# Kernel optimization log

Measured on AMD Instinct MI355X. Metric: run time of the kernel, lower is better.

## Reference

```python
import jax, jax.numpy as jnp
import numpy as np

B, L, F, D, T = 8, 400, 128, 256, 256
H = D + T            # deberta hidden_size = transfo_dim + dense_dim
NH = 8               # num_attention_heads
HD = H // NH         # head dim
BUCKETS = 600        # position_buckets == max_relative_positions
P = 2 * BUCKETS      # rel-embedding table rows

def mish(x):
    return x * jnp.tanh(jax.nn.softplus(x))

def layer_norm(x, g, b, eps=1e-7):
    m = x.mean(-1, keepdims=True)
    v = jnp.var(x, axis=-1, keepdims=True)
    return (x - m) / jnp.sqrt(v + eps) * g + b

def _rel_buckets(n, bucket=BUCKETS, max_pos=BUCKETS):
    # DeBERTa-v2 build_relative_position + make_log_bucket_position (static, numpy)
    ids = np.arange(n)
    rel = ids[:, None] - ids[None, :]
    mid = bucket // 2
    sign = np.sign(rel)
    abs_pos = np.where((rel < mid) & (rel > -mid), mid - 1, np.abs(rel))
    log_pos = np.ceil(np.log(abs_pos / mid) / np.log((max_pos - 1) / mid) * (mid - 1)) + mid
    bpos = np.where(abs_pos <= mid, rel, (log_pos * sign).astype(np.int64))
    c2p = np.clip(bpos + bucket, 0, 2 * bucket - 1).astype(np.int32)
    p2c = np.clip(-bpos + bucket, 0, 2 * bucket - 1).astype(np.int32)
    return jnp.asarray(c2p), jnp.asarray(p2c)

def _encoder(feats, mask, c2p_pos, p2c_pos, p):
    # one DebertaV2 layer with disentangled attention (share_att_key=True, pos_att_type=[c2p,p2c])
    (rel_emb, rel_g, rel_b, wq, bq, wk, bk, wv, bv,
     wo, bo, ln1g, ln1b, wi, bi, wout, bout, ln2g, ln2b) = p
    Bq, Lq, _ = feats.shape
    rel = layer_norm(rel_emb, rel_g, rel_b)                       # norm_rel_ebd='layer_norm'
    q = (feats @ wq + bq).reshape(Bq, Lq, NH, HD)
    k = (feats @ wk + bk).reshape(Bq, Lq, NH, HD)
    v = (feats @ wv + bv).reshape(Bq, Lq, NH, HD)
    pq = (rel @ wq + bq).reshape(P, NH, HD)                       # shared att key/query projs
    pk = (rel @ wk + bk).reshape(P, NH, HD)
    scale = np.float32(1.0 / np.sqrt(HD * 3))                     # scale_factor = 1 + 2 pos terms
    scores = jnp.einsum('blhd,bmhd->bhlm', q, k) * scale
    idx = jnp.arange(Lq)[:, None]
    c2p = jnp.einsum('blhd,phd->bhlp', q, pk)                     # [B,h,L,P]
    scores = scores + c2p[:, :, idx, c2p_pos] * scale             # gather c2p bias
    p2c = jnp.einsum('bmhd,phd->bhmp', k, pq)                     # [B,h,L,P]
    scores = scores + jnp.swapaxes(p2c[:, :, idx, p2c_pos], -1, -2) * scale
    valid = (mask[:, None, :, None] != 0) & (mask[:, None, None, :] != 0)
    scores = jnp.where(valid, scores, jnp.finfo(scores.dtype).min)
    probs = jax.nn.softmax(scores, axis=-1)
    ctx = jnp.einsum('bhlm,bmhd->blhd', probs, v).reshape(Bq, Lq, H)
    h1 = layer_norm(ctx @ wo + bo + feats, ln1g, ln1b)            # SelfOutput (residual)
    inter = mish(h1 @ wi + bi)                                    # intermediate, act=Mish
    return layer_norm(inter @ wout + bout, ln2g, ln2b)            # custom Output: skip residual, dim T

def _att_pool(x, w):
    xw = x * w
    return xw.sum(1) / (w.sum(1) + 1e-6), xw.max(1)

def _forward(x, w_mlp, b_mlp, w_cnn, b_cnn, rel_emb, rel_g, rel_b, wq, bq, wk, bk, wv, bv,
             wo, bo, ln1g, ln1b, wi, bi, wout, bout, ln2g, ln2b,
             w_bow1, b_bow1, w_bow2, b_bow2, w_ext1, b_ext1, w_ext2, b_ext2,
             w_org1, b_org1, w_org2, b_org2):
    f1 = mish(x @ w_mlp + b_mlp)                                  # [B,L,D]
    f2 = jax.nn.relu(jax.lax.conv_general_dilated(
        f1, w_cnn, (1,), 'SAME', dimension_numbers=('NWC', 'WIO', 'NWC')) + b_cnn)
    feats = jnp.concatenate([f1, f2], -1)                         # [B,L,H]
    kidney = x[:, :, 2:4].max(-1)
    masks = jnp.stack([x[:, :, 4], kidney, x[:, :, 0], x[:, :, 1]])  # bowel,kidney,liver,spleen [4,B,L]
    c2p_pos, p2c_pos = _rel_buckets(x.shape[1])
    params = (rel_emb, rel_g, rel_b, wq, bq, wk, bk, wv, bv,
              wo, bo, ln1g, ln1b, wi, bi, wout, bout, ln2g, ln2b)
    outs = jax.vmap(lambda m, pp: _encoder(feats, m, c2p_pos, p2c_pos, pp))(masks, params)  # [4,B,L,T]
    att, mx = jax.vmap(_att_pool)(outs, masks[..., None])         # [4,B,T] each
    pooled = jnp.concatenate([att, mx], -1)                       # [4,B,2T]
    mean = feats.mean(1)
    fmax = feats.max(1)
    lb = mish(pooled[0] @ w_bow1 + b_bow1) @ w_bow2 + b_bow2      # [B,1]
    le = mish(jnp.concatenate([mean, fmax], -1) @ w_ext1 + b_ext1) @ w_ext2 + b_ext2  # [B,1]
    ho = mish(jnp.einsum('obf,ofd->obd', pooled[1:], w_org1) + b_org1[:, None])
    lo = jnp.einsum('obd,odc->obc', ho, w_org2) + b_org2[:, None]  # [3,B,3] kidney,liver,spleen
    logits = jnp.concatenate([lb, le, lo[0], lo[1], lo[2]], -1)   # [B,11]
    return logits, jnp.zeros(x.shape[0], x.dtype)

def setup_inputs() -> dict:
    key = jax.random.key(0)
    ks = iter(jax.random.split(key, 64))
    nrm = lambda shape: jax.random.normal(next(ks), shape, jnp.float32) * 0.02
    inp = {}
    inp['x'] = jax.random.uniform(next(ks), (B, L, F), jnp.float32)  # positive: used as soft masks
    inp['w_mlp'] = nrm((F, D)); inp['b_mlp'] = jnp.zeros((D,), jnp.float32)
    inp['w_cnn'] = nrm((3, D, T)); inp['b_cnn'] = jnp.zeros((T,), jnp.float32)
    inp['rel_emb'] = nrm((4, P, H))
    inp['rel_g'] = jnp.ones((4, H), jnp.float32); inp['rel_b'] = jnp.zeros((4, H), jnp.float32)
    for n in ['wq', 'wk', 'wv', 'wo', 'wi']:
        inp[n] = nrm((4, H, H))
    for n in ['bq', 'bk', 'bv', 'bo', 'bi']:
        inp[n] = jnp.zeros((4, H), jnp.float32)
    inp['wout'] = nrm((4, H, T)); inp['bout'] = jnp.zeros((4, T), jnp.float32)
    inp['ln1g'] = jnp.ones((4, H), jnp.float32); inp['ln1b'] = jnp.zeros((4, H), jnp.float32)
    inp['ln2g'] = jnp.ones((4, T), jnp.float32); inp['ln2b'] = jnp.zeros((4, T), jnp.float32)
    inp['w_bow1'] = nrm((2 * T, D)); inp['b_bow1'] = jnp.zeros((D,), jnp.float32)
    inp['w_bow2'] = nrm((D, 1)); inp['b_bow2'] = jnp.zeros((1,), jnp.float32)
    inp['w_ext1'] = nrm((2 * H, D)); inp['b_ext1'] = jnp.zeros((D,), jnp.float32)
    inp['w_ext2'] = nrm((D, 1)); inp['b_ext2'] = jnp.zeros((1,), jnp.float32)
    inp['w_org1'] = nrm((3, 2 * T, D)); inp['b_org1'] = jnp.zeros((3, D), jnp.float32)
    inp['w_org2'] = nrm((3, D, 3)); inp['b_org2'] = jnp.zeros((3, 3), jnp.float32)
    return inp

def reference(x, w_mlp, b_mlp, w_cnn, b_cnn, rel_emb, rel_g, rel_b, wq, bq, wk, bk, wv, bv,
              wo, bo, ln1g, ln1b, wi, bi, wout, bout, ln2g, ln2b,
              w_bow1, b_bow1, w_bow2, b_bow2, w_ext1, b_ext1, w_ext2, b_ext2,
              w_org1, b_org1, w_org2, b_org2):
    return _forward(x, w_mlp, b_mlp, w_cnn, b_cnn, rel_emb, rel_g, rel_b, wq, bq, wk, bk, wv, bv,
                    wo, bo, ln1g, ln1b, wi, bi, wout, bout, ln2g, ln2b,
                    w_bow1, b_bow1, w_bow2, b_bow2, w_ext1, b_ext1, w_ext2, b_ext2,
                    w_org1, b_org1, w_org2, b_org2)
```

## Files before the change

### kernel.cpp

```cpp
#include <hip/hip_runtime.h>
#include <math.h>


typedef __attribute__((ext_vector_type(8))) short bf16x8;
typedef __attribute__((ext_vector_type(4))) float f32x4;
typedef __attribute__((ext_vector_type(4))) unsigned int u32x4;
typedef __attribute__((ext_vector_type(4))) unsigned short us4;

__device__ __forceinline__ float mishf(float x) {
    float sp = fmaxf(x, 0.f) + log1pf(expf(-fabsf(x)));
    return x * tanhf(sp);
}

__device__ __forceinline__ unsigned short f2bf(float f) {
    unsigned int u = __float_as_uint(f);
    u = (u + 0x7fffu + ((u >> 16) & 1u)) >> 16;
    return (unsigned short)u;
}
__device__ __forceinline__ float bf2f(unsigned short h) {
    return __uint_as_float(((unsigned int)h) << 16);
}

__device__ __forceinline__ void gll16(const unsigned short* g, unsigned short* l) {
    __builtin_amdgcn_global_load_lds(
        (const __attribute__((address_space(1))) void*)g,
        (__attribute__((address_space(3))) void*)l, 16, 0, 0);
}

template<int EPI>
__global__ __launch_bounds__(256) void gemm_bias(
    const float* __restrict__ A, const float* __restrict__ Bm,
    const float* __restrict__ bias, float* __restrict__ C2,
    unsigned short* __restrict__ fhi, unsigned short* __restrict__ flo,
    int M, int N, int K, int ldc)
{
    __shared__ float As[16][68];
    __shared__ float Bs[16][68];
    int bm = blockIdx.y << 6, bn = blockIdx.x << 6;
    int tid = threadIdx.x;
    int tm = (tid >> 4) << 2, tn = (tid & 15) << 2;
    int ar = tid >> 2, ac4 = (tid & 3) << 2;
    int br = tid >> 4, bc4 = (tid & 15) << 2;
    float acc[4][4] = {};
    for (int k0 = 0; k0 < K; k0 += 16) {
        float4 av = make_float4(0.f, 0.f, 0.f, 0.f);
        if (bm + ar < M)
            av = *(const float4*)&A[(long long)(bm + ar) * K + k0 + ac4];
        As[ac4][ar] = av.x; As[ac4 + 1][ar] = av.y;
        As[ac4 + 2][ar] = av.z; As[ac4 + 3][ar] = av.w;
        *(float4*)&Bs[br][bc4] =
            *(const float4*)&Bm[(long long)(k0 + br) * N + bn + bc4];
        __syncthreads();
        #pragma unroll
        for (int kk = 0; kk < 16; ++kk) {
            float4 a4 = *(const float4*)&As[kk][tm];
            float4 b4 = *(const float4*)&Bs[kk][tn];
            acc[0][0] += a4.x * b4.x; acc[0][1] += a4.x * b4.y;
            acc[0][2] += a4.x * b4.z; acc[0][3] += a4.x * b4.w;
            acc[1][0] += a4.y * b4.x; acc[1][1] += a4.y * b4.y;
            acc[1][2] += a4.y * b4.z; acc[1][3] += a4.y * b4.w;
            acc[2][0] += a4.z * b4.x; acc[2][1] += a4.z * b4.y;
            acc[2][2] += a4.z * b4.z; acc[2][3] += a4.z * b4.w;
            acc[3][0] += a4.w * b4.x; acc[3][1] += a4.w * b4.y;
            acc[3][2] += a4.w * b4.z; acc[3][3] += a4.w * b4.w;
        }
        __syncthreads();
    }
    #pragma unroll
    for (int i = 0; i < 4; ++i) {
        int r = bm + tm + i;
        if (r < M) {
            float v[4];
            #pragma unroll
            for (int q = 0; q < 4; ++q) {
                v[q] = acc[i][q] + bias[bn + tn + q];
                if (EPI == 1) v[q] = mishf(v[q]);
            }
            float4 o; o.x = v[0]; o.y = v[1]; o.z = v[2]; o.w = v[3];
            int rr2 = (r / 400) * 402 + (r % 400) + 1;
            *(float4*)&C2[(long long)rr2 * 256 + bn + tn] = o;
            us4 ph, pl;
            #pragma unroll
            for (int q = 0; q < 4; ++q) {
                unsigned short hh = f2bf(v[q]);
                ph[q] = hh;
                pl[q] = f2bf(v[q] - bf2f(hh));
            }
            *(us4*)&fhi[(long long)r * ldc + bn + tn] = ph;
            *(us4*)&flo[(long long)r * ldc + bn + tn] = pl;
        }
    }
}

template<int EPI, bool GATHER, int AMODE, bool SPLIT, int MT, bool GLL,
         int XLV, bool OUTLO>
__global__ __launch_bounds__(256) void gemm_mfma(
    const float* __restrict__ A,
    const unsigned short* __restrict__ Ahi, const unsigned short* __restrict__ Alo,
    const unsigned short* __restrict__ Bth, const unsigned short* __restrict__ Btl,
    const float* __restrict__ bias, float* __restrict__ C,
    int M, int K, int lda, int ldc, const int* __restrict__ gidx,
    unsigned short* __restrict__ Chi, unsigned short* __restrict__ Clo,
    int ldhl, int nhl,
    unsigned short* __restrict__ vthi, unsigned short* __restrict__ vtlo,
    long long zA, int zB, int zBias, int zC, int zChi, int zVt)
{
    constexpr int AI = MT / 32;
    constexpr int STR = GLL ? 32 : 40;
    __shared__ unsigned short Ah[MT * STR];
    __shared__ unsigned short Al[(XLV == 3) ? MT * STR : 16];
    __shared__ unsigned short Bh[128 * STR];
    __shared__ unsigned short Bl[(XLV == 3) ? 128 * STR : 16];

    long long zz = blockIdx.z;
    if (AMODE == 0) A += zz * zA;
    else { Ahi += zz * zA; Alo += zz * zA; }
    Bth  += zz * (long long)zB;  Btl += zz * (long long)zB;
    bias += zz * (long long)zBias;
    C    += zz * (long long)zC;
    if (SPLIT) {
        Chi += zz * (long long)zChi; Clo += zz * (long long)zChi;
        vthi += zz * (long long)zVt; vtlo += zz * (long long)zVt;
    }

    int bm = blockIdx.y * MT, bn = blockIdx.x << 7;
    int tid = threadIdx.x;
    int lane = tid & 63, wid = tid >> 6;
    int wm = wid >> 1, wn = wid & 1;
    int fr = lane & 15, kg = (lane >> 4) << 3;

    const unsigned short *aSrcH = nullptr, *aSrcL = nullptr;
    const unsigned short *bSrcH0 = nullptr, *bSrcL0 = nullptr;
    const unsigned short *bSrcH1 = nullptr, *bSrcL1 = nullptr;
    unsigned short *dstAh = nullptr, *dstAl = nullptr;
    unsigned short *dstBh0 = nullptr, *dstBl0 = nullptr;
    unsigned short *dstBh1 = nullptr, *dstBl1 = nullptr;
    bool doA = false;
    if (GLL) {
        int seg = (lane & 3) << 3;
        if (wid < MT / 16) {
            doA = true;
            int grow = bm + wid * 16 + (lane >> 2);
            grow = grow < M ? grow : (M - 1);
            long long arw = GATHER ? (long long)gidx[grow] : (long long)grow;
            aSrcH = Ahi + arw * lda + seg;
            aSrcL = Alo + arw * lda + seg;
            dstAh = &Ah[wid * 512];
            dstAl = &Al[(XLV == 3) ? wid * 512 : 0];
        }
        int br0 = bn + wid * 16 + (lane >> 2);
        int br1 = bn + (4 + wid) * 16 + (lane >> 2);
        bSrcH0 = Bth + (long long)br0 * K + seg;
        bSrcH1 = Bth + (long long)br1 * K + seg;
        bSrcL0 = Btl + (long long)br0 * K + seg;
        bSrcL1 = Btl + (long long)br1 * K + seg;
        dstBh0 = &Bh[wid * 512];       dstBh1 = &Bh[(4 + wid) * 512];
        dstBl0 = &Bl[(XLV == 3) ? wid * 512 : 0];
        dstBl1 = &Bl[(XLV == 3) ? (4 + wid) * 512 : 0];
    }

    int ar = tid >> 2, akc = (tid & 3) << 3;
    int bnr = tid >> 1, bkc = (tid & 1) << 4;
    bool astage = ar < MT;
    long long arow = 0; bool avalid = false;
    if (!GLL && astage) {
        int gr = bm + ar;
        avalid = gr < M;
        if (GATHER) arow = avalid ? (long long)gidx[gr] : 0;
        else        arow = avalid ? (long long)gr : 0;
    }

    f32x4 acc[AI][4] = {};

    for (int k0 = 0; k0 < K; k0 += 32) {
        if (GLL) {
            if (doA) {
                gll16(aSrcH + k0, dstAh);
                if (XLV == 3) gll16(aSrcL + k0, dstAl);
            }
            gll16(bSrcH0 + k0, dstBh0);
            gll16(bSrcH1 + k0, dstBh1);
            if (XLV == 3) {
                gll16(bSrcL0 + k0, dstBl0);
                gll16(bSrcL1 + k0, dstBl1);
            }
        } else {
            if (astage) {
                if (AMODE == 0) {
                    float vv[8];
                    if (avalid) {
                        float4 v0 = *(const float4*)&A[arow * lda + k0 + akc];
                        float4 v1 = *(const float4*)&A[arow * lda + k0 + akc + 4];
                        vv[0] = v0.x; vv[1] = v0.y; vv[2] = v0.z; vv[3] = v0.w;
                        vv[4] = v1.x; vv[5] = v1.y; vv[6] = v1.z; vv[7] = v1.w;
                    } else {
                        #pragma unroll
                        for (int e = 0; e < 8; ++e) vv[e] = 0.f;
                    }
                    union { unsigned short u[8]; u32x4 v; } ph, pl;
                    #pragma unroll
                    for (int e = 0; e < 8; ++e) {
                        unsigned short h = f2bf(vv[e]);
                        ph.u[e] = h;
                        pl.u[e] = f2bf(vv[e] - bf2f(h));
                    }
                    *(u32x4*)&Ah[ar * STR + akc] = ph.v;
                    if (XLV == 3) *(u32x4*)&Al[ar * STR + akc] = pl.v;
                } else {
                    u32x4 zv = {0u, 0u, 0u, 0u};
                    u32x4 vh = zv, vl = zv;
                    if (avalid) {
                        vh = *(const u32x4*)&Ahi[arow * lda + k0 + akc];
                        if (XLV == 3) vl = *(const u32x4*)&Alo[arow * lda + k0 + akc];
                    }
                    *(u32x4*)&Ah[ar * STR + akc] = vh;
                    if (XLV == 3) *(u32x4*)&Al[ar * STR + akc] = vl;
                }
            }
            long long boff = (long long)(bn + bnr) * K + k0 + bkc;
            *(u32x4*)&Bh[bnr * STR + bkc]     = *(const u32x4*)&Bth[boff];
            *(u32x4*)&Bh[bnr * STR + bkc + 8] = *(const u32x4*)&Bth[boff + 8];
            if (XLV == 3) {
                *(u32x4*)&Bl[bnr * STR + bkc]     = *(const u32x4*)&Btl[boff];
                *(u32x4*)&Bl[bnr * STR + bkc + 8] = *(const u32x4*)&Btl[boff + 8];
            }
        }
        __syncthreads();

        bf16x8 af[AI], alf[AI], bfj[4], blf[4];
        #pragma unroll
        for (int i = 0; i < AI; ++i) {
            int row = (MT == 64 ? wm * 32 + i * 16 : wm * 16) + fr;
            af[i]  = *(const bf16x8*)&Ah[row * STR + kg];
            if (XLV == 3) alf[i] = *(const bf16x8*)&Al[row * STR + kg];
        }
        #pragma unroll
        for (int j = 0; j < 4; ++j) {
            int row = wn * 64 + j * 16 + fr;
            bfj[j] = *(const bf16x8*)&Bh[row * STR + kg];
            if (XLV == 3) blf[j] = *(const bf16x8*)&Bl[row * STR + kg];
        }
        #pragma unroll
        for (int i = 0; i < AI; ++i)
        #pragma unroll
        for (int j = 0; j < 4; ++j) {
            acc[i][j] = __builtin_amdgcn_mfma_f32_16x16x32_bf16(af[i], bfj[j], acc[i][j], 0, 0, 0);
            if (XLV == 3) {
                acc[i][j] = __builtin_amdgcn_mfma_f32_16x16x32_bf16(af[i],  blf[j], acc[i][j], 0, 0, 0);
                acc[i][j] = __builtin_amdgcn_mfma_f32_16x16x32_bf16(alf[i], bfj[j], acc[i][j], 0, 0, 0);
            }
        }
        __syncthreads();
    }

    #pragma unroll
    for (int i = 0; i < AI; ++i) {
        int rbase = bm + (MT == 64 ? wm * 32 + i * 16 : wm * 16) + ((lane >> 4) << 2);
        #pragma unroll
        for (int j = 0; j < 4; ++j) {
            int ccol = bn + wn * 64 + j * 16 + fr;
            float bv = bias[ccol];
            #pragma unroll
            for (int r = 0; r < 4; ++r) {
                int row = rbase + r;
                if (row < M) {
                    float val = acc[i][j][r] + bv;
                    if (EPI == 1) val = mishf(val);
                    if (EPI == 2) val = fmaxf(val, 0.f);
                    if (SPLIT) {
                        unsigned short hh = f2bf(val);
                        if (ccol < nhl) {
                            Chi[(long long)row * ldhl + ccol] = hh;
                            if (OUTLO)
                                Clo[(long long)row * ldhl + ccol] = f2bf(val - bf2f(hh));
                        } else {
                            int bb = row / 400, m = row - bb * 400;
                            long long vi = ((long long)(bb * 512 + (ccol - 1024))) * 416 + m;
                            vthi[vi] = hh;
                            if (OUTLO)
                                vtlo[vi] = f2bf(val - bf2f(hh));
                        }
                    } else {
                        C[(long long)row * ldc + ccol] = val;
                    }
                }
            }
        }
    }
}

__global__ __launch_bounds__(256) void prep_wqkv(
    const float* __restrict__ wq, const float* __restrict__ wk,
    const float* __restrict__ wv,
    unsigned short* __restrict__ whi, unsigned short* __restrict__ wlo,
    int obase, int total, int wloEn)
{
    int idx = blockIdx.x * 256 + threadIdx.x;
    if (idx >= total) return;
    int o = obase + idx / 786432;
    int rem = idx % 786432;
    int n = rem >> 9, k = rem & 511;
    int sel = n >> 9, col = n & 511;
    const float* W = sel == 0 ? wq : (sel == 1 ? wk : wv);
    float v = W[(long long)o * 262144 + k * 512 + col];
    unsigned short h = f2bf(v);
    whi[idx] = h;
    if (wloEn) wlo[idx] = f2bf(v - bf2f(h));
}

__global__ __launch_bounds__(256) void prep_woiw(
    const float* __restrict__ wo, const float* __restrict__ wi,
    const float* __restrict__ wout,
    unsigned short* __restrict__ whi, unsigned short* __restrict__ wlo,
    int obase, int total, int wloEn)
{
    int idx = blockIdx.x * 256 + threadIdx.x;
    if (idx >= total) return;
    int o = obase + idx / 655360;
    int rem = idx % 655360;
    float v;
    if (rem < 262144) {
        int n = rem >> 9, k = rem & 511;
        v = wo[(long long)o * 262144 + k * 512 + n];
    } else if (rem < 524288) {
        int nk = rem - 262144;
        int n = nk >> 9, k = nk & 511;
        v = wi[(long long)o * 262144 + k * 512 + n];
    } else {
        int nk = rem - 524288;
        int n = nk >> 9, k = nk & 511;
        v = wout[(long long)o * 131072 + k * 256 + n];
    }
    unsigned short h = f2bf(v);
    whi[idx] = h;
    if (wloEn) wlo[idx] = f2bf(v - bf2f(h));
}

__global__ __launch_bounds__(256) void prep_wcnn(
    const float* __restrict__ w,
    unsigned short* __restrict__ whi, unsigned short* __restrict__ wlo)
{
    int idx = blockIdx.x * 256 + threadIdx.x;
    if (idx >= 256 * 768) return;
    int n = idx / 768, k = idx % 768;
    float v = w[k * 256 + n];
    unsigned short h = f2bf(v);
    whi[idx] = h;
    wlo[idx] = f2bf(v - bf2f(h));
}

__global__ __launch_bounds__(256) void setup_kernel(
    const float* __restrict__ x,
    const float* __restrict__ bq, const float* __restrict__ bk,
    const float* __restrict__ bv,
    float* __restrict__ mk, int* __restrict__ relT, int* __restrict__ convidx,
    float* __restrict__ f1pad, float* __restrict__ bqkv,
    unsigned short* __restrict__ vt_hi, unsigned short* __restrict__ vt_lo,
    int nOrg)
{
    int i = blockIdx.x * 256 + threadIdx.x;
    if (i < 3200) {
        const float* xr = x + (long long)i * 128;
        mk[i] = xr[4];
        mk[3200 + i] = fmaxf(xr[2], xr[3]);
        mk[6400 + i] = xr[0];
        mk[9600 + i] = xr[1];
        convidx[i] = (i / 400) * 402 + (i % 400);
    }
    int j = i - 3200;
    if (j >= 0 && j < 799) {
        int rel = j - 399;
        int sgn = (rel > 0) - (rel < 0);
        int ab = (rel < 300 && rel > -300) ? 299 : (rel < 0 ? -rel : rel);
        long long bpos;
        if (ab <= 300) bpos = rel;
        else {
            double lp = ceil(log((double)ab / 300.0) / log(599.0 / 300.0) * 299.0) + 300.0;
            bpos = (long long)lp * sgn;
        }
        long long c2p = bpos + 600;
        c2p = c2p < 0 ? 0 : (c2p > 1199 ? 1199 : c2p);
        relT[j] = (int)c2p;
    }
    int k = i - 4000;
    if (k >= 0 && k < 4096) {
        int b = k >> 9, rem = k & 511;
        int row = b * 402 + (rem < 256 ? 0 : 401);
        f1pad[(long long)row * 256 + (rem & 255)] = 0.f;
    }
    int m = i - 8100;
    if (m >= 0 && m < 6144) {
        int o = m / 1536, n = m % 1536;
        float v;
        if (n < 512) v = bq[o * 512 + n];
        else if (n < 1024) v = bk[o * 512 + n - 512];
        else v = bv[o * 512 + n - 1024];
        bqkv[m] = v;
    }
    int v = i - 14244;
    if (v >= 0 && v < nOrg * 65536) {
        int og = v >> 16, rem = v & 65535;
        int vb = rem & 32767;
        int row = vb >> 3, c = vb & 7;
        unsigned int* p = (unsigned int*)((rem < 32768) ? vt_hi : vt_lo);
        p[(long long)og * 851968 + row * 208 + 200 + c] = 0u;
    }
}

template<bool RES, int HD, int OSPL>
__global__ __launch_bounds__(256) void ln2_kernel(
    const float* __restrict__ X,
    const unsigned short* __restrict__ Rhi, const unsigned short* __restrict__ Rlo,
    const float* __restrict__ g, const float* __restrict__ be,
    float* __restrict__ Y,
    unsigned short* __restrict__ Yhi, unsigned short* __restrict__ Ylo,
    int rows, int rpo)
{
    constexpr int EPL = HD / 64;
    int wv = threadIdx.x >> 6, lane = threadIdx.x & 63;
    long long row = (long long)blockIdx.x * 4 + wv;
    if (row >= rows) return;
    int o = (int)(row / rpo);
    long long rrow = row % rpo;
    const float* x = X + row * HD;
    float v[EPL];
    #pragma unroll
    for (int q = 0; q < EPL / 4; ++q) {
        float4 a = *(const float4*)&x[lane * EPL + q * 4];
        v[q*4+0] = a.x; v[q*4+1] = a.y; v[q*4+2] = a.z; v[q*4+3] = a.w;
        if (RES) {
            us4 rh = *(const us4*)&Rhi[rrow * HD + lane * EPL + q * 4];
            us4 rl = *(const us4*)&Rlo[rrow * HD + lane * EPL + q * 4];
            #pragma unroll
            for (int e = 0; e < 4; ++e) v[q*4+e] += bf2f(rh[e]) + bf2f(rl[e]);
        }
    }
    float s = 0.f;
    #pragma unroll
    for (int e = 0; e < EPL; ++e) s += v[e];
    #pragma unroll
    for (int d = 1; d < 64; d <<= 1) s += __shfl_xor(s, d, 64);
    float mean = s * (1.f / HD);
    float s2 = 0.f;
    #pragma unroll
    for (int e = 0; e < EPL; ++e) { float d0 = v[e] - mean; s2 += d0 * d0; }
    #pragma unroll
    for (int d = 1; d < 64; d <<= 1) s2 += __shfl_xor(s2, d, 64);
    float inv = 1.f / sqrtf(s2 * (1.f / HD) + 1e-7f);
    #pragma unroll
    for (int q = 0; q < EPL / 4; ++q) {
        int c = lane * EPL + q * 4;
        float4 gg = *(const float4*)&g[o * HD + c];
        float4 bb = *(const float4*)&be[o * HD + c];
        float ov[4];
        ov[0] = (v[q*4+0] - mean) * inv * gg.x + bb.x;
        ov[1] = (v[q*4+1] - mean) * inv * gg.y + bb.y;
        ov[2] = (v[q*4+2] - mean) * inv * gg.z + bb.z;
        ov[3] = (v[q*4+3] - mean) * inv * gg.w + bb.w;
        if (OSPL == 1 || OSPL == 2) {
            us4 ph, pl;
            #pragma unroll
            for (int e = 0; e < 4; ++e) {
                unsigned short hh = f2bf(ov[e]);
                ph[e] = hh;
                pl[e] = f2bf(ov[e] - bf2f(hh));
            }
            *(us4*)&Yhi[row * HD + c] = ph;
            if (OSPL == 1) *(us4*)&Ylo[row * HD + c] = pl;
        } else {
            float4 of; of.x = ov[0]; of.y = ov[1]; of.z = ov[2]; of.w = ov[3];
            *(float4*)&Y[row * HD + c] = of;
        }
    }
}

__global__ __launch_bounds__(64) void attn_kernel(
    const unsigned short* __restrict__ qk_hi, const unsigned short* __restrict__ qk_lo,
    const unsigned short* __restrict__ vt_hi, const unsigned short* __restrict__ vt_lo,
    const unsigned short* __restrict__ pkg_hi, const unsigned short* __restrict__ pkg_lo,
    const float* __restrict__ mask,
    unsigned short* __restrict__ ctxh, unsigned short* __restrict__ ctxl)
{
    const float scale = 0.07216878364870322f;
    const float NEGMIN = -3.402823466e38f;
    int lin = blockIdx.x + 25 * (blockIdx.y + 8 * blockIdx.z);
    int gz = gridDim.z;
    int xcd = lin & 7, within = lin >> 3;
    int g = within / 25, lt = within - g * 25;
    int combo = xcd * gz + g;
    int h = combo & 7, z = combo >> 3;
    int b = z & 7, o = z >> 3;
    qk_hi  += (long long)o * 3276800;
    vt_hi  += (long long)o * 1703936;
    pkg_hi += (long long)o * 818176;
    mask   += o * 3200;
    ctxh   += (long long)o * 1638400;

    int l0 = lt * 16;
    int lane = threadIdx.x;
    int fr = lane & 15, kg8 = (lane >> 4) << 3, g4 = (lane >> 4) << 2;
    int rowS = lane >> 2, segS = (lane & 3) << 3;

    __shared__ unsigned short PB[12 * 512];
    __shared__ float T2c[16 * 36];
    __shared__ float T3c[32 * 20];
    __shared__ unsigned short Sth[16 * 40];

    bf16x8 qf[2];
    {
        long long base = ((long long)(b * 400 + l0 + fr)) * 1024 + h * 64 + kg8;
        #pragma unroll
        for (int kk = 0; kk < 2; ++kk)
            qf[kk] = *(const bf16x8*)(qk_hi + base + kk * 32);
    }
    float wlv_r[4], ms[4], ls[4];
    #pragma unroll
    for (int r = 0; r < 4; ++r) {
        wlv_r[r] = mask[b * 400 + l0 + g4 + r];
        ms[r] = -INFINITY;
        ls[r] = 0.f;
    }
    f32x4 O[4] = {};
    long long vtbase = ((long long)(b * 512 + h * 64)) * 416;

    for (int mt = 0; mt < 13; ++mt) {
        int m0 = mt * 32;
        int D0 = l0 - m0 + 368;
        __syncthreads();
        #pragma unroll
        for (int c = 0; c < 3; ++c) {
            int dd = D0 + c * 16 + rowS;
            dd = dd < 0 ? 0 : (dd > 798 ? 798 : dd);
            const unsigned short* gb = pkg_hi + (long long)dd * 1024 + h * 64 + segS;
            #pragma unroll
            for (int kk = 0; kk < 2; ++kk) {
                gll16(gb + kk * 32,       &PB[(c * 2 + kk) * 512]);
                gll16(gb + 512 + kk * 32, &PB[(6 + c * 2 + kk) * 512]);
            }
        }
        __syncthreads();
        bf16x8 kf[2][2];
        #pragma unroll
        for (int jf = 0; jf < 2; ++jf) {
            int kr = m0 + jf * 16 + fr;
            kr = kr < 400 ? kr : 399;
            long long base = ((long long)(b * 400 + kr)) * 1024 + 512 + h * 64 + kg8;
            #pragma unroll
            for (int kk = 0; kk < 2; ++kk)
                kf[jf][kk] = *(const bf16x8*)(qk_hi + base + kk * 32);
        }
        bf16x8 vf[4];
        #pragma unroll
        for (int f = 0; f < 4; ++f) {
            long long a = vtbase + (long long)(f * 16 + fr) * 416 + m0 + kg8;
            vf[f] = *(const bf16x8*)&vt_hi[a];
        }
        float wm_c[2];
        #pragma unroll
        for (int cf = 0; cf < 2; ++cf) {
            int mg = m0 + cf * 16 + fr;
            mg = mg < 400 ? mg : 399;
            wm_c[cf] = mask[b * 400 + mg];
        }
        __builtin_amdgcn_s_setprio(1);
        f32x4 aT1[2] = {};
        #pragma unroll
        for (int jf = 0; jf < 2; ++jf)
        #pragma unroll
        for (int kk = 0; kk < 2; ++kk)
            aT1[jf] = __builtin_amdgcn_mfma_f32_16x16x32_bf16(qf[kk], kf[jf][kk], aT1[jf], 0, 0, 0);
        f32x4 aT2[3] = {};
        #pragma unroll
        for (int c = 0; c < 3; ++c)
        #pragma unroll
        for (int kk = 0; kk < 2; ++kk) {
            bf16x8 bf = *(const bf16x8*)&PB[(6 + c * 2 + kk) * 512 + fr * 32 + kg8];
            aT2[c] = __builtin_amdgcn_mfma_f32_16x16x32_bf16(qf[kk], bf, aT2[c], 0, 0, 0);
        }
        f32x4 aT3[2][2] = {};
        #pragma unroll
        for (int jf = 0; jf < 2; ++jf)
        #pragma unroll
        for (int ci = 0; ci < 2; ++ci) {
            int c = ci + (jf ^ 1);
            #pragma unroll
            for (int kk = 0; kk < 2; ++kk) {
                bf16x8 bf = *(const bf16x8*)&PB[(c * 2 + kk) * 512 + fr * 32 + kg8];
                aT3[jf][ci] = __builtin_amdgcn_mfma_f32_16x16x32_bf16(kf[jf][kk], bf, aT3[jf][ci], 0, 0, 0);
            }
        }
        __builtin_amdgcn_s_setprio(0);
        #pragma unroll
        for (int c = 0; c < 3; ++c)
        #pragma unroll
        for (int r = 0; r < 4; ++r) {
            int i = g4 + r;
            int d = c * 16 + fr - i;
            if ((unsigned)d < 32u)
                T2c[i * 36 + d] = aT2[c][r];
        }
        #pragma unroll
        for (int jf = 0; jf < 2; ++jf)
        #pragma unroll
        for (int ci = 0; ci < 2; ++ci) {
            int c = ci + (jf ^ 1);
            #pragma unroll
            for (int r = 0; r < 4; ++r) {
                int j3 = jf * 16 + g4 + r;
                int d2 = c * 16 + fr + j3 - 31;
                if ((unsigned)d2 < 16u)
                    T3c[j3 * 20 + d2] = aT3[jf][ci][r];
            }
        }
        float sc0[4], sc1[4];
        #pragma unroll
        for (int r = 0; r < 4; ++r) {
            int i = g4 + r;
            {
                int j = fr;
                bool jv = (m0 + j) < 400;
                sc0[r] = !jv ? -INFINITY :
                    ((wlv_r[r] != 0.f && wm_c[0] != 0.f) ?
                     (aT1[0][r] + T2c[i * 36 + 31 - j] + T3c[j * 20 + i]) * scale : NEGMIN);
            }
            {
                int j = 16 + fr;
                bool jv = (m0 + j) < 400;
                sc1[r] = !jv ? -INFINITY :
                    ((wlv_r[r] != 0.f && wm_c[1] != 0.f) ?
                     (aT1[1][r] + T2c[i * 36 + 31 - j] + T3c[j * 20 + i]) * scale : NEGMIN);
            }
        }
        float corr[4];
        #pragma unroll
        for (int r = 0; r < 4; ++r) {
            float mx = fmaxf(sc0[r], sc1[r]);
            #pragma unroll
            for (int d = 1; d < 16; d <<= 1) mx = fmaxf(mx, __shfl_xor(mx, d, 64));
            float mn = fmaxf(ms[r], mx);
            corr[r] = __expf(ms[r] - mn);
            ms[r] = mn;
            float p0 = __expf(sc0[r] - mn), p1 = __expf(sc1[r] - mn);
            float rs = p0 + p1;
            #pragma unroll
            for (int d = 1; d < 16; d <<= 1) rs += __shfl_xor(rs, d, 64);
            ls[r] = ls[r] * corr[r] + rs;
            int i = g4 + r;
            Sth[i * 40 + fr] = f2bf(p0);
            Sth[i * 40 + 16 + fr] = f2bf(p1);
        }
        #pragma unroll
        for (int f = 0; f < 4; ++f)
        #pragma unroll
        for (int r = 0; r < 4; ++r) O[f][r] *= corr[r];
        bf16x8 Pha = *(const bf16x8*)&Sth[fr * 40 + kg8];
        __builtin_amdgcn_s_setprio(1);
        #pragma unroll
        for (int f = 0; f < 4; ++f)
            O[f] = __builtin_amdgcn_mfma_f32_16x16x32_bf16(Pha, vf[f], O[f], 0, 0, 0);
        __builtin_amdgcn_s_setprio(0);
    }
    #pragma unroll
    for (int f = 0; f < 4; ++f) {
        int colg = h * 64 + f * 16 + fr;
        #pragma unroll
        for (int r = 0; r < 4; ++r) {
            int lg = l0 + g4 + r;
            float val = O[f][r] / ls[r];
            long long idx = ((long long)(b * 400 + lg)) * 512 + colg;
            ctxh[idx] = f2bf(val);
        }
    }
}

__global__ __launch_bounds__(256) void pool_part(
    const float* __restrict__ in, long long inOStride,
    const float* __restrict__ mk, float* __restrict__ pp)
{
    int bi = blockIdx.x, c = blockIdx.y, t = threadIdx.x;
    int o = bi >> 3, b = bi & 7;
    int l0 = c * 31, l1 = min(400, l0 + 31);
    const float* ib = in + (long long)o * inOStride + (long long)(b * 400) * 256;
    const float* mkb = mk + o * 3200 + b * 400;
    float s = 0.f, mx = -INFINITY, sw = 0.f;
    for (int l = l0; l < l1; ++l) {
        float wv = mkb[l];
        float v = ib[(long long)l * 256 + t] * wv;
        s += v; mx = fmaxf(mx, v); sw += wv;
    }
    long long base = (long long)(c * gridDim.x + bi) * 514;
    pp[base + t] = s;
    pp[base + 256 + t] = mx;
    if (t == 0) pp[base + 512] = sw;
}

__global__ __launch_bounds__(256) void pool_merge(
    const float* __restrict__ pp, float* __restrict__ pooled, int nBI)
{
    int bi = blockIdx.x, t = threadIdx.x;
    float s = 0.f, mx = -INFINITY, sw = 0.f;
    for (int c = 0; c < 13; ++c) {
        long long base = (long long)(c * nBI + bi) * 514;
        s += pp[base + t];
        mx = fmaxf(mx, pp[base + 256 + t]);
        sw += pp[base + 512];
    }
    int o = bi >> 3, b = bi & 7;
    pooled[o * 4096 + b * 512 + t] = s / (sw + 1e-6f);
    pooled[o * 4096 + b * 512 + 256 + t] = mx;
}

__global__ __launch_bounds__(512) void mm_part(
    const unsigned short* __restrict__ fh, const unsigned short* __restrict__ fl,
    float* __restrict__ mmp)
{
    int b = blockIdx.x, c = blockIdx.y, t = threadIdx.x;
    int l0 = c * 31, l1 = min(400, l0 + 31);
    float s = 0.f, mx = -INFINITY;
    for (int l = l0; l < l1; ++l) {
        long long idx = ((long long)(b * 400 + l)) * 512 + t;
        float v = bf2f(fh[idx]) + bf2f(fl[idx]);
        s += v; mx = fmaxf(mx, v);
    }
    long long base = (long long)(c * 8 + b) * 1024;
    mmp[base + t] = s;
    mmp[base + 512 + t] = mx;
}

__global__ __launch_bounds__(512) void mm_merge(
    const float* __restrict__ mmp, float* __restrict__ mm)
{
    int b = blockIdx.x, t = threadIdx.x;
    float s = 0.f, mx = -INFINITY;
    for (int c = 0; c < 13; ++c) {
        long long base = (long long)(c * 8 + b) * 1024;
        s += mmp[base + t];
        mx = fmaxf(mx, mmp[base + 512 + t]);
    }
    mm[b * 1024 + t] = s / 400.f;
    mm[b * 1024 + 512 + t] = mx;
}

__global__ __launch_bounds__(256) void heads_kernel(
    const float* __restrict__ pooled, const float* __restrict__ mm,
    const float* __restrict__ w_bow1, const float* __restrict__ b_bow1,
    const float* __restrict__ w_bow2, const float* __restrict__ b_bow2,
    const float* __restrict__ w_ext1, const float* __restrict__ b_ext1,
    const float* __restrict__ w_ext2, const float* __restrict__ b_ext2,
    const float* __restrict__ w_org1, const float* __restrict__ b_org1,
    const float* __restrict__ w_org2, const float* __restrict__ b_org2,
    float* __restrict__ out)
{
    int b = blockIdx.x, role = blockIdx.y;
    int t = threadIdx.x;
    __shared__ float inb[1024];
    __shared__ float red[256];
    __shared__ float hid[256];
    if (role == 0) {
        inb[t] = pooled[b * 512 + t];
        inb[256 + t] = pooled[b * 512 + 256 + t];
        __syncthreads();
        float acc = b_bow1[t];
        for (int j = 0; j < 512; ++j) acc += inb[j] * w_bow1[j * 256 + t];
        red[t] = mishf(acc) * w_bow2[t];
        __syncthreads();
        for (int s = 128; s; s >>= 1) { if (t < s) red[t] += red[t + s]; __syncthreads(); }
        if (t == 0) out[b * 11 + 0] = red[0] + b_bow2[0];
    } else if (role == 1) {
        inb[t] = mm[b * 1024 + t];
        inb[256 + t] = mm[b * 1024 + 256 + t];
        inb[512 + t] = mm[b * 1024 + 512 + t];
        inb[768 + t] = mm[b * 1024 + 768 + t];
        __syncthreads();
        float acc = b_ext1[t];
        for (int j = 0; j < 1024; ++j) acc += inb[j] * w_ext1[j * 256 + t];
        red[t] = mishf(acc) * w_ext2[t];
        __syncthreads();
        for (int s = 128; s; s >>= 1) { if (t < s) red[t] += red[t + s]; __syncthreads(); }
        if (t == 0) { out[b * 11 + 1] = red[0] + b_ext2[0]; out[88 + b] = 0.f; }
    } else {
        int i = role - 2;
        inb[t] = pooled[((1 + i) * 8 + b) * 512 + t];
        inb[256 + t] = pooled[((1 + i) * 8 + b) * 512 + 256 + t];
        __syncthreads();
        float acc = b_org1[i * 256 + t];
        for (int j = 0; j < 512; ++j)
            acc += inb[j] * w_org1[((long long)i * 512 + j) * 256 + t];
        hid[t] = mishf(acc);
        __syncthreads();
        for (int c = 0; c < 3; ++c) {
            red[t] = hid[t] * w_org2[(i * 256 + t) * 3 + c];
            __syncthreads();
            for (int s = 128; s; s >>= 1) { if (t < s) red[t] += red[t + s]; __syncthreads(); }
            if (t == 0) out[b * 11 + 2 + i * 3 + c] = red[0] + b_org2[i * 3 + c];
            __syncthreads();
        }
    }
}

extern "C" void kernel_launch(void* const* d_in, const int* in_sizes, int n_in,
                              void* d_out, int out_size, void* d_ws, size_t ws_size,
                              hipStream_t stream)
{
    const float* x      = (const float*)d_in[0];
    const float* w_mlp  = (const float*)d_in[1];
    const float* b_mlp  = (const float*)d_in[2];
    const float* w_cnn  = (const float*)d_in[3];
    const float* b_cnn  = (const float*)d_in[4];
    const float* rel_emb= (const float*)d_in[5];
    const float* rel_g  = (const float*)d_in[6];
    const float* rel_b  = (const float*)d_in[7];
    const float* wq     = (const float*)d_in[8];
    const float* wk     = (const float*)d_in[9];
    const float* wv     = (const float*)d_in[10];
    const float* wo     = (const float*)d_in[11];
    const float* wi     = (const float*)d_in[12];
    const float* bq     = (const float*)d_in[13];
    const float* bk     = (const float*)d_in[14];
    const float* bv     = (const float*)d_in[15];
    const float* bo     = (const float*)d_in[16];
    const float* bi     = (const float*)d_in[17];
    const float* wout   = (const float*)d_in[18];
    const float* bout   = (const float*)d_in[19];
    const float* ln1g   = (const float*)d_in[20];
    const float* ln1b   = (const float*)d_in[21];
    const float* ln2g   = (const float*)d_in[22];
    const float* ln2b   = (const float*)d_in[23];
    const float* w_bow1 = (const float*)d_in[24];
    const float* b_bow1 = (const float*)d_in[25];
    const float* w_bow2 = (const float*)d_in[26];
    const float* b_bow2 = (const float*)d_in[27];
    const float* w_ext1 = (const float*)d_in[28];
    const float* b_ext1 = (const float*)d_in[29];
    const float* w_ext2 = (const float*)d_in[30];
    const float* b_ext2 = (const float*)d_in[31];
    const float* w_org1 = (const float*)d_in[32];
    const float* b_org1 = (const float*)d_in[33];
    const float* w_org2 = (const float*)d_in[34];
    const float* b_org2 = (const float*)d_in[35];

    float* ws = (float*)d_ws;
    float* outf = (float*)d_out;
    const bool big = ws_size >= 143012736ull;

    if (big) {
        unsigned short* featsh = (unsigned short*)(ws + 0);
        unsigned short* featsl = (unsigned short*)(ws + 819200);
        float* ctxR     = ws + 1638400;
        float* f1pad    = ctxR;
        unsigned short* ctxh = (unsigned short*)ctxR;
        unsigned short* ctxl = (unsigned short*)(ws + 4915200);
        float* qkA_f    = ws + 8192000;
        float* qkB_f    = ws + 14745600;
        unsigned short* qkA = (unsigned short*)qkA_f;
        unsigned short* qkB = (unsigned short*)qkB_f;
        unsigned short* rellnh = (unsigned short*)qkA_f;
        unsigned short* rellnl = (unsigned short*)(ws + 8192000 + 1228800);
        unsigned short* vtA = (unsigned short*)(ws + 21299200);
        unsigned short* vtB = (unsigned short*)(ws + 24707072);
        unsigned short* pkgA = (unsigned short*)(ws + 28114944);
        unsigned short* pkgB = (unsigned short*)(ws + 29751296);
        unsigned short* whiA = (unsigned short*)(ws + 31387648);
        unsigned short* wloA = (unsigned short*)(ws + 32960512);
        unsigned short* wcnn_hi = (unsigned short*)(ws + 35188736);
        unsigned short* wcnn_lo = (unsigned short*)(ws + 35287040);
        float* bqkvb   = ws + 35385344;
        float* masksb  = ws + 35391488;
        float* pooledb = ws + 35404288;
        float* mmb     = ws + 35420672;
        int*   relidx  = (int*)(ws + 35428864);
        int*   convidx = (int*)(ws + 35429664);
        float* poolpart= ws + 35432864;
        float* mmpart  = ws + 35646688;
        float* tmp_all   = qkA_f;
        unsigned short* h1h = (unsigned short*)qkB_f;
        unsigned short* interh = (unsigned short*)qkA_f;
        float* outenc_all = (float*)vtA;
        float* outln_all  = ctxR;
        unsigned short* whiB_all = whiA;
        unsigned short* wloB_all = wloA;

        gemm_bias<1><<<dim3(4, 50), 256, 0, stream>>>(
            x, w_mlp, b_mlp, f1pad, featsh, featsl, 3200, 256, 128, 512);
        setup_kernel<<<1080, 256, 0, stream>>>(x, bq, bk, bv, masksb, relidx, convidx,
                                               f1pad, bqkvb, vtA, vtB, 4);
        prep_wcnn<<<768, 256, 0, stream>>>(w_cnn, wcnn_hi, wcnn_lo);
        gemm_mfma<2, true, 0, true, 32, false, 3, true><<<dim3(2, 100), 256, 0, stream>>>(
            f1pad, nullptr, nullptr, wcnn_hi, wcnn_lo, b_cnn, nullptr,
            3200, 768, 256, 0, convidx, featsh + 256, featsl + 256, 512, 1 << 30,
            nullptr, nullptr, 0, 0, 0, 0, 0, 0);

        ln2_kernel<false, 512, 1><<<1200, 256, 0, stream>>>(
            rel_emb, nullptr, nullptr, rel_g, rel_b, nullptr, rellnh, rellnl, 4800, 1200);
        prep_wqkv<<<12288, 256, 0, stream>>>(wq, wk, wv, whiA, wloA, 0, 3145728, 0);
        gemm_mfma<0, true, 1, true, 64, true, 1, false><<<dim3(8, 13, 4), 256, 0, stream>>>(
            nullptr, rellnh, rellnl, whiA, wloA, bqkvb, nullptr, 799, 512, 512, 0, relidx,
            pkgA, pkgB, 1024, 1024, nullptr, nullptr,
            614400, 786432, 1536, 0, 818176, 0);
        gemm_mfma<0, false, 1, true, 64, true, 1, false><<<dim3(12, 50, 4), 256, 0, stream>>>(
            nullptr, featsh, featsl, whiA, wloA, bqkvb, nullptr, 3200, 512, 512, 0, nullptr,
            qkA, qkB, 1024, 1024, vtA, vtB,
            0, 786432, 1536, 0, 3276800, 1703936);
        prep_woiw<<<10240, 256, 0, stream>>>(wo, wi, wout, whiB_all, wloB_all,
                                             0, 2621440, 0);
        attn_kernel<<<dim3(25, 8, 32), 64, 0, stream>>>(qkA, qkB, vtA, vtB,
            pkgA, pkgB, masksb, ctxh, ctxl);
        gemm_mfma<0, false, 1, false, 32, true, 1, false><<<dim3(4, 100, 4), 256, 0, stream>>>(
            nullptr, ctxh, ctxl, whiB_all, wloB_all, bo, tmp_all,
            3200, 512, 512, 512, nullptr, nullptr, nullptr, 0, 0, nullptr, nullptr,
            1638400, 655360, 512, 1638400, 0, 0);
        ln2_kernel<true, 512, 2><<<3200, 256, 0, stream>>>(
            tmp_all, featsh, featsl, ln1g, ln1b, nullptr, h1h, nullptr, 12800, 3200);
        gemm_mfma<1, false, 1, true, 32, true, 1, false><<<dim3(4, 100, 4), 256, 0, stream>>>(
            nullptr, h1h, nullptr, whiB_all + 262144, wloB_all + 262144, bi, nullptr,
            3200, 512, 512, 0, nullptr, interh, nullptr, 512, 1 << 30, nullptr, nullptr,
            1638400, 655360, 512, 0, 1638400, 0);
        gemm_mfma<0, false, 1, false, 32, true, 1, false><<<dim3(2, 100, 4), 256, 0, stream>>>(
            nullptr, interh, nullptr, whiB_all + 524288, wloB_all + 524288, bout, outenc_all,
            3200, 512, 512, 256, nullptr, nullptr, nullptr, 0, 0, nullptr, nullptr,
            1638400, 655360, 256, 819200, 0, 0);
        ln2_kernel<false, 256, 0><<<3200, 256, 0, stream>>>(
            outenc_all, nullptr, nullptr, ln2g, ln2b, outln_all, nullptr, nullptr,
            12800, 3200);

        pool_part<<<dim3(32, 13), 256, 0, stream>>>(outln_all, 819200, masksb, poolpart);
        pool_merge<<<32, 256, 0, stream>>>(poolpart, pooledb, 32);
        mm_part<<<dim3(8, 13), 512, 0, stream>>>(featsh, featsl, mmpart);
        mm_merge<<<8, 512, 0, stream>>>(mmpart, mmb);
        heads_kernel<<<dim3(8, 5), 256, 0, stream>>>(pooledb, mmb,
            w_bow1, b_bow1, w_bow2, b_bow2, w_ext1, b_ext1, w_ext2, b_ext2,
            w_org1, b_org1, w_org2, b_org2, outf);
        return;
    }

    unsigned short* featsh = (unsigned short*)(ws + 0);
    unsigned short* featsl = (unsigned short*)(ws + 819200);
    float* ctxR    = ws + 1638400;
    float* f1pad   = ctxR;
    unsigned short* ctxh = (unsigned short*)ctxR;
    unsigned short* ctxl = (unsigned short*)(ws + 1638400 + 819200);
    float* qkvA_f  = ws + 3276800;
    float* qkvB_f  = ws + 4915200;
    unsigned short* qkv_hi = (unsigned short*)qkvA_f;
    unsigned short* qkv_lo = (unsigned short*)qkvB_f;
    unsigned short* rellnh = (unsigned short*)qkvB_f;
    unsigned short* rellnl = (unsigned short*)(ws + 4915200 + 307200);
    unsigned short* pkg_hi = (unsigned short*)(ws + 6553600);
    unsigned short* pkg_lo = (unsigned short*)(ws + 6963200);
    unsigned short* vt_hi  = (unsigned short*)(ws + 7372800);
    unsigned short* vt_lo  = (unsigned short*)(ws + 8224768);
    unsigned short* whi    = (unsigned short*)(ws + 9076736);
    unsigned short* wlo    = (unsigned short*)(ws + 9469952);
    float* bqkvb   = ws + 9863168;
    float* masksb  = ws + 9869312;
    float* pooledb = ws + 9882112;
    float* mmb     = ws + 9898496;
    int*   relidx  = (int*)(ws + 9906688);
    unsigned short* wcnn_hi = (unsigned short*)(ws + 9907488);
    unsigned short* wcnn_lo = (unsigned short*)(ws + 10005792);
    int*   convidx = (int*)(ws + 10104096);
    float* poolpart= ws + 10107296;
    float* mmpart  = ws + 10160752;
    float* tmp     = qkvA_f;
    unsigned short* h1h = (unsigned short*)qkvB_f;
    unsigned short* interh = (unsigned short*)qkvA_f;
    float* outenc  = (float*)vt_hi;
    float* outln   = ctxR;

    gemm_bias<1><<<dim3(4, 50), 256, 0, stream>>>(
        x, w_mlp, b_mlp, f1pad, featsh, featsl, 3200, 256, 128, 512);
    setup_kernel<<<312, 256, 0, stream>>>(x, bq, bk, bv, masksb, relidx, convidx,
                                          f1pad, bqkvb, vt_hi, vt_lo, 1);
    prep_wcnn<<<768, 256, 0, stream>>>(w_cnn, wcnn_hi, wcnn_lo);
    gemm_mfma<2, true, 0, true, 32, false, 3, true><<<dim3(2, 100), 256, 0, stream>>>(
        f1pad, nullptr, nullptr, wcnn_hi, wcnn_lo, b_cnn, nullptr,
        3200, 768, 256, 0, convidx, featsh + 256, featsl + 256, 512, 1 << 30,
        nullptr, nullptr, 0, 0, 0, 0, 0, 0);

    for (int o = 0; o < 4; ++o) {
        ln2_kernel<false, 512, 1><<<300, 256, 0, stream>>>(
            rel_emb + (long long)o * 614400, nullptr, nullptr,
            rel_g + o * 512, rel_b + o * 512, nullptr, rellnh, rellnl, 1200, 1200);
        prep_wqkv<<<3072, 256, 0, stream>>>(wq, wk, wv, whi, wlo, o, 786432, 0);
        gemm_mfma<0, true, 1, true, 64, true, 1, false><<<dim3(8, 13), 256, 0, stream>>>(
            nullptr, rellnh, rellnl, whi, wlo, bqkvb + o * 1536, nullptr,
            799, 512, 512, 0, relidx, pkg_hi, pkg_lo, 1024, 1024, nullptr, nullptr,
            0, 0, 0, 0, 0, 0);
        gemm_mfma<0, false, 1, true, 64, true, 1, false><<<dim3(12, 50), 256, 0, stream>>>(
            nullptr, featsh, featsl, whi, wlo, bqkvb + o * 1536, nullptr,
            3200, 512, 512, 0, nullptr, qkv_hi, qkv_lo, 1024, 1024, vt_hi, vt_lo,
            0, 0, 0, 0, 0, 0);
        prep_woiw<<<2560, 256, 0, stream>>>(wo, wi, wout, whi, wlo, o, 655360, 0);
        attn_kernel<<<dim3(25, 8, 8), 64, 0, stream>>>(qkv_hi, qkv_lo, vt_hi, vt_lo,
            pkg_hi, pkg_lo, masksb + o * 3200, ctxh, ctxl);
        gemm_mfma<0, false, 1, false, 32, true, 1, false><<<dim3(4, 100), 256, 0, stream>>>(
            nullptr, ctxh, ctxl, whi, wlo, bo + o * 512, tmp,
            3200, 512, 512, 512, nullptr, nullptr, nullptr, 0, 0, nullptr, nullptr,
            0, 0, 0, 0, 0, 0);
        ln2_kernel<true, 512, 2><<<800, 256, 0, stream>>>(
            tmp, featsh, featsl, ln1g + o * 512, ln1b + o * 512, nullptr,
            h1h, nullptr, 3200, 3200);
        gemm_mfma<1, false, 1, true, 32, true, 1, false><<<dim3(4, 100), 256, 0, stream>>>(
            nullptr, h1h, nullptr, whi + 262144, wlo + 262144, bi + o * 512, nullptr,
            3200, 512, 512, 0, nullptr, interh, nullptr, 512, 1 << 30, nullptr, nullptr,
            0, 0, 0, 0, 0, 0);
        gemm_mfma<0, false, 1, false, 32, true, 1, false><<<dim3(2, 100), 256, 0, stream>>>(
            nullptr, interh, nullptr, whi + 524288, wlo + 524288, bout + o * 256, outenc,
            3200, 512, 512, 256, nullptr, nullptr, nullptr, 0, 0, nullptr, nullptr,
            0, 0, 0, 0, 0, 0);
        ln2_kernel<false, 256, 0><<<800, 256, 0, stream>>>(
            outenc, nullptr, nullptr, ln2g + o * 256, ln2b + o * 256, outln,
            nullptr, nullptr, 3200, 3200);
        pool_part<<<dim3(8, 13), 256, 0, stream>>>(outln, 0,
                                                   masksb + o * 3200, poolpart);
        pool_merge<<<8, 256, 0, stream>>>(poolpart, pooledb + o * 4096, 8);
    }

    mm_part<<<dim3(8, 13), 512, 0, stream>>>(featsh, featsl, mmpart);
    mm_merge<<<8, 512, 0, stream>>>(mmpart, mmb);
    heads_kernel<<<dim3(8, 5), 256, 0, stream>>>(pooledb, mmb,
        w_bow1, b_bow1, w_bow2, b_bow2, w_ext1, b_ext1, w_ext2, b_ext2,
        w_org1, b_org1, w_org2, b_org2, outf);
}
```

Baseline: 464.5 us.

## Software-pipeline K/V/mask register loads and rel-pos LDS tiles across iterations

```diff
diff --git a/kernel.cpp b/kernel.cpp
--- a/kernel.cpp
+++ b/kernel.cpp
@@ -523,10 +523,10 @@
     f32x4 O[4] = {};
     long long vtbase = ((long long)(b * 512 + h * 64)) * 416;
 
-    for (int mt = 0; mt < 13; ++mt) {
-        int m0 = mt * 32;
-        int D0 = l0 - m0 + 368;
-        __syncthreads();
+    bf16x8 kfn[2][2], vfn[4];
+    float wmn[2];
+    {
+        int D0 = l0 + 368;
         #pragma unroll
         for (int c = 0; c < 3; ++c) {
             int dd = D0 + c * 16 + rowS;
@@ -538,29 +538,56 @@
                 gll16(gb + 512 + kk * 32, &PB[(6 + c * 2 + kk) * 512]);
             }
         }
-        __syncthreads();
-        bf16x8 kf[2][2];
         #pragma unroll
         for (int jf = 0; jf < 2; ++jf) {
-            int kr = m0 + jf * 16 + fr;
-            kr = kr < 400 ? kr : 399;
+            int kr = jf * 16 + fr;
             long long base = ((long long)(b * 400 + kr)) * 1024 + 512 + h * 64 + kg8;
             #pragma unroll
             for (int kk = 0; kk < 2; ++kk)
-                kf[jf][kk] = *(const bf16x8*)(qk_hi + base + kk * 32);
-        }
-        bf16x8 vf[4];
-        #pragma unroll
-        for (int f = 0; f < 4; ++f) {
-            long long a = vtbase + (long long)(f * 16 + fr) * 416 + m0 + kg8;
-            vf[f] = *(const bf16x8*)&vt_hi[a];
-        }
+                kfn[jf][kk] = *(const bf16x8*)(qk_hi + base + kk * 32);
+        }
+        #pragma unroll
+        for (int f = 0; f < 4; ++f)
+            vfn[f] = *(const bf16x8*)&vt_hi[vtbase + (long long)(f * 16 + fr) * 416 + kg8];
+        #pragma unroll
+        for (int cf = 0; cf < 2; ++cf)
+            wmn[cf] = mask[b * 400 + cf * 16 + fr];
+    }
+
+    for (int mt = 0; mt < 13; ++mt) {
+        int m0 = mt * 32;
+        int D0 = l0 - m0 + 368;
+        asm volatile("s_waitcnt vmcnt(0)" ::: "memory");
+        __builtin_amdgcn_sched_barrier(0);
+        bf16x8 kf[2][2], vf[4];
         float wm_c[2];
         #pragma unroll
-        for (int cf = 0; cf < 2; ++cf) {
-            int mg = m0 + cf * 16 + fr;
-            mg = mg < 400 ? mg : 399;
-            wm_c[cf] = mask[b * 400 + mg];
+        for (int jf = 0; jf < 2; ++jf)
+        #pragma unroll
+        for (int kk = 0; kk < 2; ++kk) kf[jf][kk] = kfn[jf][kk];
+        #pragma unroll
+        for (int f = 0; f < 4; ++f) vf[f] = vfn[f];
+        wm_c[0] = wmn[0]; wm_c[1] = wmn[1];
+        if (mt < 12) {
+            int m1 = m0 + 32;
+            #pragma unroll
+            for (int jf = 0; jf < 2; ++jf) {
+                int kr = m1 + jf * 16 + fr;
+                kr = kr < 400 ? kr : 399;
+                long long base = ((long long)(b * 400 + kr)) * 1024 + 512 + h * 64 + kg8;
+                #pragma unroll
+                for (int kk = 0; kk < 2; ++kk)
+                    kfn[jf][kk] = *(const bf16x8*)(qk_hi + base + kk * 32);
+            }
+            #pragma unroll
+            for (int f = 0; f < 4; ++f)
+                vfn[f] = *(const bf16x8*)&vt_hi[vtbase + (long long)(f * 16 + fr) * 416 + m1 + kg8];
+            #pragma unroll
+            for (int cf = 0; cf < 2; ++cf) {
+                int mg = m1 + cf * 16 + fr;
+                mg = mg < 400 ? mg : 399;
+                wmn[cf] = mask[b * 400 + mg];
+            }
         }
         __builtin_amdgcn_s_setprio(1);
         f32x4 aT1[2] = {};
@@ -590,6 +617,22 @@
             }
         }
         __builtin_amdgcn_s_setprio(0);
+        if (mt < 12) {
+            __builtin_amdgcn_sched_barrier(0);
+            int D0n = D0 - 32;
+            #pragma unroll
+            for (int c = 0; c < 3; ++c) {
+                int dd = D0n + c * 16 + rowS;
+                dd = dd < 0 ? 0 : (dd > 798 ? 798 : dd);
+                const unsigned short* gb = pkg_hi + (long long)dd * 1024 + h * 64 + segS;
+                #pragma unroll
+                for (int kk = 0; kk < 2; ++kk) {
+                    gll16(gb + kk * 32,       &PB[(c * 2 + kk) * 512]);
+                    gll16(gb + 512 + kk * 32, &PB[(6 + c * 2 + kk) * 512]);
+                }
+            }
+            __builtin_amdgcn_sched_barrier(0);
+        }
         #pragma unroll
         for (int c = 0; c < 3; ++c)
         #pragma unroll
```

New measurement: 472.3 us. No clear change (+1.7%).
